# Kernel tuning notes

Hardware: AMD Instinct MI355X
Metric: run time of the kernel (lower is better)

Reference implementation:

```python
import jax, jax.numpy as jnp
import numpy as np

N = 50000      # nodes
E = 800000     # edges (avg degree 16)
INDIM = 128
OUTDIM = 64


def setup_inputs() -> dict:
    key = jax.random.key(0)
    k1, k2, k3, k4, k5 = jax.random.split(key, 5)
    h = jax.random.normal(k1, (N, INDIM), dtype=jnp.float32)
    W = jax.random.normal(k2, (INDIM, OUTDIM), dtype=jnp.float32) * 0.05
    Wa = jax.random.normal(k3, (2 * OUTDIM,), dtype=jnp.float32) * 0.05
    src = jax.random.randint(k4, (E,), 0, N)
    dst = jax.random.randint(k5, (E,), 0, N)
    return {"h": h, "W": W, "Wa": Wa, "src": src, "dst": dst}


def reference(h, W, Wa, src, dst):
    # node transform: n_mlp_layer=1, bias=False MultiLinearLayer == one linear
    z = h @ W  # [N, OUTDIM]
    # edge attention: relu(attn_linear(cat(z_src, z_dst)))
    # avoid materializing [E, 2*OUTDIM] concat: split Wa into src/dst halves
    s = z @ Wa[:OUTDIM]   # [N] src contribution
    t = z @ Wa[OUTDIM:]   # [N] dst contribution
    e = jax.nn.relu(s[src] + t[dst])  # [E]
    # segment softmax over incoming edges of each destination node
    m = jax.ops.segment_max(e, dst, num_segments=N)      # [N]
    ex = jnp.exp(e - m[dst])                             # [E]
    denom = jax.ops.segment_sum(ex, dst, num_segments=N) # [N]
    alpha = ex / denom[dst]                              # [E]
    # weighted scatter-sum aggregation of src features (dropout p=0 -> identity)
    h_out = jax.ops.segment_sum(alpha[:, None] * z[src], dst, num_segments=N)
    # batch_norm=False; final activation relu; dropout p=0 -> identity
    return jax.nn.relu(h_out)
```

## Files before the change

### kernel.cpp

```cpp
#include <hip/hip_runtime.h>
#include <math.h>

#define INDIM 128
#define OUTDIM 64
#define HK 136
#define CP 68
#define SCHUNK 2048

typedef __bf16 bf16x8 __attribute__((ext_vector_type(8)));
typedef float f32x4 __attribute__((ext_vector_type(4)));
typedef unsigned short ushortx8 __attribute__((ext_vector_type(8)));

static __device__ __forceinline__ unsigned short f2bf(float f) {
    unsigned u = __float_as_uint(f);
    u += 0x7FFFu + ((u >> 16) & 1u);
    return (unsigned short)(u >> 16);
}
static __device__ __forceinline__ float bf2f(unsigned short b) {
    return __uint_as_float((unsigned)b << 16);
}

__global__ __launch_bounds__(256) void nt_count(
    const float* __restrict__ h, const float* __restrict__ W,
    const float* __restrict__ Wa, unsigned short* __restrict__ z,
    float* __restrict__ s, float* __restrict__ t,
    const int* __restrict__ dst, int* __restrict__ bcnt,
    int N, int E, int gemm_blocks)
{
    __shared__ __align__(16) unsigned short smem[2 * 64 * HK];
    unsigned short* As = smem;
    unsigned short* Bs = smem + 64 * HK;
    float* Cs = (float*)smem;
    int tid = threadIdx.x;

    if (blockIdx.x >= gemm_blocks) {
        int* l = (int*)smem;
        l[tid] = 0;
        __syncthreads();
        int base = (blockIdx.x - gemm_blocks) * 8192;
        #pragma unroll 4
        for (int u = 0; u < 32; ++u) {
            int i = base + u * 256 + tid;
            if (i < E) atomicAdd(&l[dst[i] >> 8], 1);
        }
        __syncthreads();
        if (l[tid]) atomicAdd(bcnt + tid, l[tid]);
        return;
    }

    int node0 = blockIdx.x * 64;
    int nv = min(64, N - node0);

    {
        const float4* hg = (const float4*)(h + (size_t)node0 * INDIM);
        #pragma unroll
        for (int i = 0; i < 8; ++i) {
            int idx = i * 256 + tid;
            int n = idx >> 5, j = idx & 31;
            float4 v = (n < nv) ? hg[n * 32 + j] : make_float4(0.f, 0.f, 0.f, 0.f);
            ushort4 b = make_ushort4(f2bf(v.x), f2bf(v.y), f2bf(v.z), f2bf(v.w));
            *(ushort4*)&As[n * HK + j * 4] = b;
        }
    }
    {
        int n = tid & 63, kg = tid >> 6;
        const float* Wc = W + n;
        #pragma unroll
        for (int uu = 0; uu < 8; ++uu) {
            int k = kg * 32 + uu * 4;
            ushort4 b = make_ushort4(f2bf(Wc[(k + 0) * OUTDIM]),
                                     f2bf(Wc[(k + 1) * OUTDIM]),
                                     f2bf(Wc[(k + 2) * OUTDIM]),
                                     f2bf(Wc[(k + 3) * OUTDIM]));
            *(ushort4*)&Bs[n * HK + k] = b;
        }
    }
    __syncthreads();

    int wv = tid >> 6, l = tid & 63;
    int lr = l & 15, lg = l >> 4;

    f32x4 acc[4];
    #pragma unroll
    for (int nf = 0; nf < 4; ++nf) acc[nf] = (f32x4){0.f, 0.f, 0.f, 0.f};

    #pragma unroll
    for (int ks = 0; ks < 4; ++ks) {
        int k0 = ks * 32 + lg * 8;
        bf16x8 a = *(const bf16x8*)&As[(wv * 16 + lr) * HK + k0];
        #pragma unroll
        for (int nf = 0; nf < 4; ++nf) {
            bf16x8 b = *(const bf16x8*)&Bs[(nf * 16 + lr) * HK + k0];
            acc[nf] = __builtin_amdgcn_mfma_f32_16x16x32_bf16(a, b, acc[nf], 0, 0, 0);
        }
    }

    __syncthreads();

    #pragma unroll
    for (int nf = 0; nf < 4; ++nf)
        #pragma unroll
        for (int r = 0; r < 4; ++r)
            Cs[(wv * 16 + lg * 4 + r) * CP + nf * 16 + lr] = acc[nf][r];

    int row = wv * 16 + (l >> 2);
    int cq = l & 3;
    int node = node0 + row;
    float ssum = 0.f, tsum = 0.f;
    #pragma unroll
    for (int qq = 0; qq < 2; ++qq) {
        int c0 = cq * 16 + qq * 8;
        float4 ca = *(const float4*)&Cs[row * CP + c0];
        float4 cb = *(const float4*)&Cs[row * CP + c0 + 4];
        float4 wsa = *(const float4*)&Wa[c0];
        float4 wsb = *(const float4*)&Wa[c0 + 4];
        float4 wta = *(const float4*)&Wa[OUTDIM + c0];
        float4 wtb = *(const float4*)&Wa[OUTDIM + c0 + 4];
        ssum += ca.x * wsa.x + ca.y * wsa.y + ca.z * wsa.z + ca.w * wsa.w
              + cb.x * wsb.x + cb.y * wsb.y + cb.z * wsb.z + cb.w * wsb.w;
        tsum += ca.x * wta.x + ca.y * wta.y + ca.z * wta.z + ca.w * wta.w
              + cb.x * wtb.x + cb.y * wtb.y + cb.z * wtb.z + cb.w * wtb.w;
        if (node < N) {
            ushortx8 zb;
            zb[0] = f2bf(ca.x); zb[1] = f2bf(ca.y);
            zb[2] = f2bf(ca.z); zb[3] = f2bf(ca.w);
            zb[4] = f2bf(cb.x); zb[5] = f2bf(cb.y);
            zb[6] = f2bf(cb.z); zb[7] = f2bf(cb.w);
            *(ushortx8*)&z[(size_t)node * OUTDIM + c0] = zb;
        }
    }
    ssum += __shfl_xor(ssum, 1, 64);
    ssum += __shfl_xor(ssum, 2, 64);
    tsum += __shfl_xor(tsum, 1, 64);
    tsum += __shfl_xor(tsum, 2, 64);
    if (cq == 0 && node < N) {
        s[node] = ssum;
        t[node] = tsum;
    }
}

__global__ __launch_bounds__(256) void bucket_scatter(
    const int* __restrict__ src, const int* __restrict__ dst,
    const int* __restrict__ bcnt, int* __restrict__ gcursor,
    int* __restrict__ esort, int E)
{
    __shared__ int lcnt[256];
    __shared__ int loff[256];
    __shared__ int gbase[256];
    __shared__ int lcur[256];
    __shared__ int bs[256];
    __shared__ int stage[SCHUNK];
    __shared__ unsigned char bof[SCHUNK];
    int tid = threadIdx.x;
    int base = blockIdx.x * SCHUNK;
    int ne = min(SCHUNK, E - base);

    int bc = bcnt[tid];
    bs[tid] = bc;
    lcnt[tid] = 0;
    __syncthreads();
    for (int off = 1; off < 256; off <<= 1) {
        int add = (tid >= off) ? bs[tid - off] : 0;
        __syncthreads();
        bs[tid] += add;
        __syncthreads();
    }
    int bstart_own = bs[tid] - bc;

    int mys[8], myd[8];
    #pragma unroll
    for (int u = 0; u < 8; ++u) {
        int li = u * 256 + tid;
        if (li < ne) {
            mys[u] = src[base + li];
            myd[u] = dst[base + li];
            atomicAdd(&lcnt[myd[u] >> 8], 1);
        } else myd[u] = -1;
    }
    __syncthreads();

    loff[tid] = lcnt[tid];
    __syncthreads();
    for (int off = 1; off < 256; off <<= 1) {
        int add = (tid >= off) ? loff[tid - off] : 0;
        __syncthreads();
        loff[tid] += add;
        __syncthreads();
    }
    int excl = loff[tid] - lcnt[tid];
    loff[tid] = excl;
    lcur[tid] = excl;
    if (lcnt[tid] > 0)
        gbase[tid] = bstart_own + atomicAdd(gcursor + tid, lcnt[tid]);
    __syncthreads();

    #pragma unroll
    for (int u = 0; u < 8; ++u) {
        if (myd[u] >= 0) {
            int b = myd[u] >> 8;
            int p = atomicAdd(&lcur[b], 1);
            stage[p] = ((myd[u] & 255) << 24) | mys[u];
            bof[p] = (unsigned char)b;
        }
    }
    __syncthreads();

    for (int i = tid; i < ne; i += 256) {
        int b = bof[i];
        esort[gbase[b] + (i - loff[b])] = stage[i];
    }
}

__global__ __launch_bounds__(256) void bucket_fill(
    const int* __restrict__ esort, const int* __restrict__ bcnt,
    int* __restrict__ counts, int* __restrict__ offsets,
    int* __restrict__ srcs, int N)
{
    __shared__ int bs[256];
    __shared__ int cnt[256];
    __shared__ int off[256];
    __shared__ int cur[256];
    int tid = threadIdx.x;
    int b = blockIdx.x;

    int bc = bcnt[tid];
    bs[tid] = bc;
    cnt[tid] = 0;
    __syncthreads();
    for (int o = 1; o < 256; o <<= 1) {
        int add = (tid >= o) ? bs[tid - o] : 0;
        __syncthreads();
        bs[tid] += add;
        __syncthreads();
    }
    int e0 = (b > 0) ? bs[b - 1] : 0;
    int e1 = bs[b];
    int node0 = b << 8;

    for (int i = e0 + tid; i < e1; i += 256)
        atomicAdd(&cnt[((unsigned)esort[i]) >> 24], 1);
    __syncthreads();

    off[tid] = cnt[tid];
    __syncthreads();
    for (int o = 1; o < 256; o <<= 1) {
        int add = (tid >= o) ? off[tid - o] : 0;
        __syncthreads();
        off[tid] += add;
        __syncthreads();
    }
    int excl = off[tid] - cnt[tid];
    cur[tid] = excl;
    int node = node0 + tid;
    if (node < N) { counts[node] = cnt[tid]; offsets[node] = e0 + excl; }
    __syncthreads();

    for (int i = e0 + tid; i < e1; i += 256) {
        int pe = esort[i];
        int p = atomicAdd(&cur[((unsigned)pe) >> 24], 1);
        srcs[e0 + p] = pe & 0xFFFFFF;
    }
}

__global__ __launch_bounds__(256) void aggregate(
    const unsigned short* __restrict__ z, const int* __restrict__ srcs,
    const float* __restrict__ s, const float* __restrict__ t,
    const int* __restrict__ offsets, const int* __restrict__ counts,
    float* __restrict__ out, int N)
{
    int wave = threadIdx.x >> 6;
    int lane = threadIdx.x & 63;
    int node = blockIdx.x * 4 + wave;
    if (node >= N) return;
    int start = offsets[node];
    int deg = counts[node];
    size_t orow = (size_t)node * OUTDIM + lane;
    if (deg == 0) { out[orow] = 0.f; return; }
    float tn = t[node];

    if (deg <= 64) {
        int sn = 0; float ex = 0.f;
        if (lane < deg) {
            sn = srcs[start + lane];
            ex = __expf(fmaxf(s[sn] + tn, 0.f));
        }
        float se = ex;
        #pragma unroll
        for (int off = 32; off; off >>= 1) se += __shfl_xor(se, off, 64);

        float acc = 0.f;
        int j = 0;
        for (; j + 16 <= deg; j += 16) {
            int si[16]; float ei[16]; unsigned short ai[16];
            #pragma unroll
            for (int u = 0; u < 16; ++u) {
                si[u] = __shfl(sn, j + u, 64);
                ei[u] = __shfl(ex, j + u, 64);
            }
            #pragma unroll
            for (int u = 0; u < 16; ++u)
                ai[u] = z[(size_t)si[u] * OUTDIM + lane];
            #pragma unroll
            for (int u = 0; u < 16; ++u)
                acc += ei[u] * bf2f(ai[u]);
        }
        for (; j + 4 <= deg; j += 4) {
            int s0 = __shfl(sn, j, 64),     s1 = __shfl(sn, j + 1, 64);
            int s2 = __shfl(sn, j + 2, 64), s3 = __shfl(sn, j + 3, 64);
            float e0 = __shfl(ex, j, 64),     e1 = __shfl(ex, j + 1, 64);
            float e2 = __shfl(ex, j + 2, 64), e3 = __shfl(ex, j + 3, 64);
            float a0 = bf2f(z[(size_t)s0 * OUTDIM + lane]);
            float a1 = bf2f(z[(size_t)s1 * OUTDIM + lane]);
            float a2 = bf2f(z[(size_t)s2 * OUTDIM + lane]);
            float a3 = bf2f(z[(size_t)s3 * OUTDIM + lane]);
            acc += e0 * a0; acc += e1 * a1; acc += e2 * a2; acc += e3 * a3;
        }
        for (; j < deg; ++j) {
            int sj = __shfl(sn, j, 64);
            float ej = __shfl(ex, j, 64);
            acc += ej * bf2f(z[(size_t)sj * OUTDIM + lane]);
        }
        out[orow] = fmaxf(acc / se, 0.f);
    } else {
        float mx = 0.f;
        for (int j = lane; j < deg; j += 64) {
            int sj = srcs[start + j];
            mx = fmaxf(mx, fmaxf(s[sj] + tn, 0.f));
        }
        #pragma unroll
        for (int off = 32; off; off >>= 1) mx = fmaxf(mx, __shfl_xor(mx, off, 64));
        float se = 0.f;
        for (int j = lane; j < deg; j += 64) {
            int sj = srcs[start + j];
            se += __expf(fmaxf(s[sj] + tn, 0.f) - mx);
        }
        #pragma unroll
        for (int off = 32; off; off >>= 1) se += __shfl_xor(se, off, 64);
        float acc = 0.f;
        for (int j = 0; j < deg; ++j) {
            int sj = srcs[start + j];
            float ej = __expf(fmaxf(s[sj] + tn, 0.f) - mx);
            acc += ej * bf2f(z[(size_t)sj * OUTDIM + lane]);
        }
        out[orow] = fmaxf(acc / se, 0.f);
    }
}

extern "C" void kernel_launch(void* const* d_in, const int* in_sizes, int n_in,
                              void* d_out, int out_size, void* d_ws, size_t ws_size,
                              hipStream_t stream) {
    const float* h  = (const float*)d_in[0];
    const float* W  = (const float*)d_in[1];
    const float* Wa = (const float*)d_in[2];
    const int* src  = (const int*)d_in[3];
    const int* dst  = (const int*)d_in[4];
    int N = in_sizes[0] / INDIM;
    int E = in_sizes[3];
    float* out = (float*)d_out;
    int nbuck = (N + 255) >> 8;

    char* ws = (char*)d_ws;
    unsigned short* z = (unsigned short*)ws;  ws += (size_t)N * OUTDIM * 2;
    float* s       = (float*)ws;  ws += (size_t)N * 4;
    float* t       = (float*)ws;  ws += (size_t)N * 4;
    int*   srcs    = (int*)ws;    ws += (size_t)E * 4;
    int*   counts  = (int*)ws;    ws += (size_t)N * 4;
    int*   offsets = (int*)ws;    ws += (size_t)N * 4;
    int*   esort   = (int*)ws;    ws += (size_t)E * 4;
    int*   bcnt    = (int*)ws;    ws += 256 * 4;
    int*   gcursor = (int*)ws;    ws += 256 * 4;

    int gemm_blocks = (N + 63) / 64;
    int count_blocks = (E + 8191) / 8192;

    hipMemsetAsync(bcnt, 0, 512 * sizeof(int), stream);

    nt_count<<<gemm_blocks + count_blocks, 256, 0, stream>>>(
        h, W, Wa, z, s, t, dst, bcnt, N, E, gemm_blocks);
    bucket_scatter<<<(E + SCHUNK - 1) / SCHUNK, 256, 0, stream>>>(
        src, dst, bcnt, gcursor, esort, E);
    bucket_fill<<<nbuck, 256, 0, stream>>>(esort, bcnt, counts, offsets, srcs, N);
    aggregate<<<(N + 3) / 4, 256, 0, stream>>>(z, srcs, s, t, offsets, counts, out, N);
}
```

Measured before the change: 147.6 us.

## Aggregate with half-wave per node, two features per lane, LDS edge staging

The aggregate kernel now assigns 32 lanes per destination node, with each lane handling two bf16 features through a 4-byte load. Edge source indices and exp weights are staged in shared memory in chunks of 64, which replaces the shuffle broadcasts and merges the high-degree path into a single loop. The goal is to double the number of nodes per wave and widen the gather loads, so more independent gathers are in flight. The max-subtraction for high-degree nodes is removed, which could overflow for large logits, and the uniform shared-memory reads add some LDS traffic.

```diff
diff --git a/kernel.cpp b/kernel.cpp
--- a/kernel.cpp
+++ b/kernel.cpp
@@ -268,82 +268,62 @@
     const int* __restrict__ offsets, const int* __restrict__ counts,
     float* __restrict__ out, int N)
 {
-    int wave = threadIdx.x >> 6;
-    int lane = threadIdx.x & 63;
-    int node = blockIdx.x * 4 + wave;
+    __shared__ int   ls[8][64];
+    __shared__ float le[8][64];
+    int hw = threadIdx.x >> 5;
+    int lane = threadIdx.x & 31;
+    int node = blockIdx.x * 8 + hw;
     if (node >= N) return;
     int start = offsets[node];
     int deg = counts[node];
-    size_t orow = (size_t)node * OUTDIM + lane;
-    if (deg == 0) { out[orow] = 0.f; return; }
-    float tn = t[node];
-
-    if (deg <= 64) {
-        int sn = 0; float ex = 0.f;
-        if (lane < deg) {
-            sn = srcs[start + lane];
-            ex = __expf(fmaxf(s[sn] + tn, 0.f));
-        }
-        float se = ex;
-        #pragma unroll
-        for (int off = 32; off; off >>= 1) se += __shfl_xor(se, off, 64);
-
-        float acc = 0.f;
-        int j = 0;
-        for (; j + 16 <= deg; j += 16) {
-            int si[16]; float ei[16]; unsigned short ai[16];
-            #pragma unroll
-            for (int u = 0; u < 16; ++u) {
-                si[u] = __shfl(sn, j + u, 64);
-                ei[u] = __shfl(ex, j + u, 64);
+    float2 acc = make_float2(0.f, 0.f);
+
+    if (deg > 0) {
+        float tn = t[node];
+        float se = 0.f;
+        for (int c0 = 0; c0 < deg; c0 += 64) {
+            int cn = min(64, deg - c0);
+            float pe = 0.f;
+            if (lane < cn) {
+                int sj = srcs[start + c0 + lane];
+                float e = __expf(fmaxf(s[sj] + tn, 0.f));
+                ls[hw][lane] = sj; le[hw][lane] = e; pe += e;
+            }
+            if (lane + 32 < cn) {
+                int sj = srcs[start + c0 + lane + 32];
+                float e = __expf(fmaxf(s[sj] + tn, 0.f));
+                ls[hw][lane + 32] = sj; le[hw][lane + 32] = e; pe += e;
             }
             #pragma unroll
-            for (int u = 0; u < 16; ++u)
-                ai[u] = z[(size_t)si[u] * OUTDIM + lane];
-            #pragma unroll
-            for (int u = 0; u < 16; ++u)
-                acc += ei[u] * bf2f(ai[u]);
-        }
-        for (; j + 4 <= deg; j += 4) {
-            int s0 = __shfl(sn, j, 64),     s1 = __shfl(sn, j + 1, 64);
-            int s2 = __shfl(sn, j + 2, 64), s3 = __shfl(sn, j + 3, 64);
-            float e0 = __shfl(ex, j, 64),     e1 = __shfl(ex, j + 1, 64);
-            float e2 = __shfl(ex, j + 2, 64), e3 = __shfl(ex, j + 3, 64);
-            float a0 = bf2f(z[(size_t)s0 * OUTDIM + lane]);
-            float a1 = bf2f(z[(size_t)s1 * OUTDIM + lane]);
-            float a2 = bf2f(z[(size_t)s2 * OUTDIM + lane]);
-            float a3 = bf2f(z[(size_t)s3 * OUTDIM + lane]);
-            acc += e0 * a0; acc += e1 * a1; acc += e2 * a2; acc += e3 * a3;
-        }
-        for (; j < deg; ++j) {
-            int sj = __shfl(sn, j, 64);
-            float ej = __shfl(ex, j, 64);
-            acc += ej * bf2f(z[(size_t)sj * OUTDIM + lane]);
-        }
-        out[orow] = fmaxf(acc / se, 0.f);
-    } else {
-        float mx = 0.f;
-        for (int j = lane; j < deg; j += 64) {
-            int sj = srcs[start + j];
-            mx = fmaxf(mx, fmaxf(s[sj] + tn, 0.f));
-        }
-        #pragma unroll
-        for (int off = 32; off; off >>= 1) mx = fmaxf(mx, __shfl_xor(mx, off, 64));
-        float se = 0.f;
-        for (int j = lane; j < deg; j += 64) {
-            int sj = srcs[start + j];
-            se += __expf(fmaxf(s[sj] + tn, 0.f) - mx);
-        }
-        #pragma unroll
-        for (int off = 32; off; off >>= 1) se += __shfl_xor(se, off, 64);
-        float acc = 0.f;
-        for (int j = 0; j < deg; ++j) {
-            int sj = srcs[start + j];
-            float ej = __expf(fmaxf(s[sj] + tn, 0.f) - mx);
-            acc += ej * bf2f(z[(size_t)sj * OUTDIM + lane]);
-        }
-        out[orow] = fmaxf(acc / se, 0.f);
-    }
+            for (int off = 16; off; off >>= 1) pe += __shfl_xor(pe, off, 32);
+            se += pe;
+
+            int j = 0;
+            for (; j + 8 <= cn; j += 8) {
+                int si[8]; float ei[8]; ushort2 ai[8];
+                #pragma unroll
+                for (int u = 0; u < 8; ++u) { si[u] = ls[hw][j + u]; ei[u] = le[hw][j + u]; }
+                #pragma unroll
+                for (int u = 0; u < 8; ++u)
+                    ai[u] = *(const ushort2*)&z[(size_t)si[u] * OUTDIM + lane * 2];
+                #pragma unroll
+                for (int u = 0; u < 8; ++u) {
+                    acc.x += ei[u] * bf2f(ai[u].x);
+                    acc.y += ei[u] * bf2f(ai[u].y);
+                }
+            }
+            for (; j < cn; ++j) {
+                int sj = ls[hw][j]; float ej = le[hw][j];
+                ushort2 a = *(const ushort2*)&z[(size_t)sj * OUTDIM + lane * 2];
+                acc.x += ej * bf2f(a.x);
+                acc.y += ej * bf2f(a.y);
+            }
+        }
+        float inv = 1.f / se;
+        acc.x = fmaxf(acc.x * inv, 0.f);
+        acc.y = fmaxf(acc.y * inv, 0.f);
+    }
+    *(float2*)&out[(size_t)node * OUTDIM + lane * 2] = acc;
 }
 
 extern "C" void kernel_launch(void* const* d_in, const int* in_sizes, int n_in,
@@ -380,5 +360,5 @@
     bucket_scatter<<<(E + SCHUNK - 1) / SCHUNK, 256, 0, stream>>>(
         src, dst, bcnt, gcursor, esort, E);
     bucket_fill<<<nbuck, 256, 0, stream>>>(esort, bcnt, counts, offsets, srcs, N);
-    aggregate<<<(N + 3) / 4, 256, 0, stream>>>(z, srcs, s, t, offsets, counts, out, N);
-}
+    aggregate<<<(N + 7) / 8, 256, 0, stream>>>(z, srcs, s, t, offsets, counts, out, N);
+}
```

New measurement: 141.6 us. -4.0%, faster.
